# Kernel tuning notes

Hardware: AMD Instinct MI355X
Metric: run time of the kernel (lower is better)

## Reference

```python
import jax, jax.numpy as jnp
import numpy as np

N, E = 50000, 600000
IN, H, C = 128, 8, 32
HC = H * C
LAT, OUT, NCOM = 32, 64, 30
BN_EPS = 1e-5
NEG_SLOPE = 0.2


def setup_inputs() -> dict:
    key = jax.random.key(0)
    ks = jax.random.split(key, 32)
    f32 = jnp.float32
    def rn(i, shape, s=0.05):
        return jax.random.normal(ks[i], shape, f32) * s
    inp = {
        'x': jax.random.normal(ks[0], (N, IN), f32),
        'eps': jax.random.normal(ks[1], (N, LAT), f32),
        'edge_index': jax.random.randint(ks[2], (2, E), 0, N, jnp.int32),
        # GAT layer 1 (in -> H*C)
        'gat1_W': rn(3, (IN, HC)), 'gat1_asrc': rn(4, (H, C)), 'gat1_adst': rn(5, (H, C)), 'gat1_b': jnp.zeros((HC,), f32),
        'bn1_g': jnp.ones((HC,), f32), 'bn1_b': jnp.zeros((HC,), f32),
        # GAT layer 2 (H*C -> H*C)
        'gat2_W': rn(6, (HC, HC)), 'gat2_asrc': rn(7, (H, C)), 'gat2_adst': rn(8, (H, C)), 'gat2_b': jnp.zeros((HC,), f32),
        'bn2_g': jnp.ones((HC,), f32), 'bn2_b': jnp.zeros((HC,), f32),
        # GAT layer 3 (H*C -> H*C)
        'gat3_W': rn(9, (HC, HC)), 'gat3_asrc': rn(10, (H, C)), 'gat3_adst': rn(11, (H, C)), 'gat3_b': jnp.zeros((HC,), f32),
        'bn3_g': jnp.ones((HC,), f32), 'bn3_b': jnp.zeros((HC,), f32),
        # heads
        'res_W': rn(12, (IN, HC)), 'res_b': jnp.zeros((HC,), f32),
        'mu_W': rn(13, (HC, LAT)), 'mu_b': jnp.zeros((LAT,), f32),
        'lv_W': rn(14, (HC, LAT)), 'lv_b': jnp.zeros((LAT,), f32),
        'dec_W': rn(15, (LAT, OUT)), 'dec_b': jnp.zeros((OUT,), f32),
        'aux_W': rn(16, (HC, NCOM)), 'aux_b': jnp.zeros((NCOM,), f32),
    }
    return inp


def gat_conv(x, src, dst, W, asrc, adst, b):
    # PyG GATConv (concat=True, self-loops already in src/dst, lin bias=False)
    n = x.shape[0]
    h = (x @ W).reshape(n, H, C)                      # [N,H,C]
    a_s = jnp.einsum('nhc,hc->nh', h, asrc)           # [N,H]
    a_d = jnp.einsum('nhc,hc->nh', h, adst)
    e = jax.nn.leaky_relu(a_s[src] + a_d[dst], NEG_SLOPE)  # [E,H]
    m = jax.ops.segment_max(e, dst, num_segments=n)        # per-dest softmax (stable)
    p = jnp.exp(e - m[dst])
    s = jax.ops.segment_sum(p, dst, num_segments=n)
    alpha = p / (s[dst] + 1e-16)                      # [E,H]
    out = jax.ops.segment_sum(h[src] * alpha[:, :, None], dst, num_segments=n)
    return out.reshape(n, HC) + b


def batch_norm(x, g, b):
    mu = x.mean(0)
    var = x.var(0)  # biased var, as torch BN uses for normalization
    return (x - mu) * jax.lax.rsqrt(var + BN_EPS) * g + b


def reference(x, eps, edge_index,
              gat1_W, gat1_asrc, gat1_adst, gat1_b, bn1_g, bn1_b,
              gat2_W, gat2_asrc, gat2_adst, gat2_b, bn2_g, bn2_b,
              gat3_W, gat3_asrc, gat3_adst, gat3_b, bn3_g, bn3_b,
              res_W, res_b, mu_W, mu_b, lv_W, lv_b, dec_W, dec_b, aux_W, aux_b):
    loops = jnp.arange(N, dtype=edge_index.dtype)
    src = jnp.concatenate([edge_index[0], loops])
    dst = jnp.concatenate([edge_index[1], loops])

    residual = x @ res_W + res_b
    h = jax.nn.relu(batch_norm(gat_conv(x, src, dst, gat1_W, gat1_asrc, gat1_adst, gat1_b), bn1_g, bn1_b))
    h = jax.nn.relu(batch_norm(gat_conv(h, src, dst, gat2_W, gat2_asrc, gat2_adst, gat2_b), bn2_g, bn2_b))
    h = jax.nn.relu(batch_norm(gat_conv(h, src, dst, gat3_W, gat3_asrc, gat3_adst, gat3_b), bn3_g, bn3_b))
    h = h + residual

    mu = h @ mu_W + mu_b
    logvar = h @ lv_W + lv_b
    z = mu + eps * jnp.exp(0.5 * logvar)   # reparameterize
    out = z @ dec_W + dec_b
    aux = h @ aux_W + aux_b
    return (out, mu, logvar, aux)
```

## Files before the change

kernel.cpp:

```cpp
#include <hip/hip_runtime.h>

#define N_NODES 50000
#define N_EDGES 600000
#define HC 256
#define NH 8
#define AGG_BLOCKS 2048
#define AGG_WAVES (AGG_BLOCKS * 4)

typedef short s8v __attribute__((ext_vector_type(8)));
typedef float f4v __attribute__((ext_vector_type(4)));
typedef _Float16 h4v __attribute__((ext_vector_type(4)));
typedef _Float16 h8v __attribute__((ext_vector_type(8)));
typedef __attribute__((address_space(1))) const unsigned int as1_cu32;
typedef __attribute__((address_space(3))) unsigned int as3_u32;

__device__ inline ushort f2bf(float f) {
  unsigned u = __float_as_uint(f);
  unsigned r = u + 0x7FFF + ((u >> 16) & 1);
  return (ushort)(r >> 16);
}

__global__ void k_init_cnt(int* __restrict__ cnt) {
  int i = blockIdx.x * 256 + threadIdx.x;
  if (i < N_NODES) cnt[i] = 1;
}

__global__ void k_count(const int* __restrict__ dstE, int* __restrict__ cnt) {
  int e = blockIdx.x * 256 + threadIdx.x;
  if (e < N_EDGES) atomicAdd(&cnt[dstE[e]], 1);
}

__global__ void k_scan_bsum(const int* __restrict__ cnt, int* __restrict__ bsum) {
  __shared__ int sd[256];
  int i = blockIdx.x * 256 + threadIdx.x;
  sd[threadIdx.x] = (i < N_NODES) ? cnt[i] : 0;
  __syncthreads();
  for (int o = 128; o > 0; o >>= 1) {
    if (threadIdx.x < o) sd[threadIdx.x] += sd[threadIdx.x + o];
    __syncthreads();
  }
  if (threadIdx.x == 0) bsum[blockIdx.x] = sd[0];
}

__global__ void k_scan_offsets(int* __restrict__ bsum, int nb) {
  __shared__ int s[256];
  int t = threadIdx.x;
  int v = (t < nb) ? bsum[t] : 0;
  s[t] = v; __syncthreads();
  for (int o = 1; o < 256; o <<= 1) {
    int x = (t >= o) ? s[t - o] : 0;
    __syncthreads();
    s[t] += x;
    __syncthreads();
  }
  if (t < nb) bsum[t] = s[t] - v;
}

__global__ void k_scan_write(const int* __restrict__ cnt, const int* __restrict__ bsum,
                             int* __restrict__ rowptr, int* __restrict__ fillptr) {
  __shared__ int s[256];
  int t = threadIdx.x;
  int i = blockIdx.x * 256 + t;
  int v = (i < N_NODES) ? cnt[i] : 0;
  s[t] = v; __syncthreads();
  for (int o = 1; o < 256; o <<= 1) {
    int x = (t >= o) ? s[t - o] : 0;
    __syncthreads();
    s[t] += x;
    __syncthreads();
  }
  int excl = s[t] - v + bsum[blockIdx.x];
  if (i < N_NODES) {
    rowptr[i] = excl;
    fillptr[i] = excl;
    if (i == N_NODES - 1) rowptr[N_NODES] = excl + v;
  }
}

__global__ void k_fill(const int* __restrict__ srcE, const int* __restrict__ dstE,
                       int* __restrict__ fillptr, int* __restrict__ srcs) {
  int i = blockIdx.x * 256 + threadIdx.x;
  if (i < N_NODES) {
    int pos = atomicAdd(&fillptr[i], 1);
    srcs[pos] = i;
  } else if (i < N_NODES + N_EDGES) {
    int e = i - N_NODES;
    int pos = atomicAdd(&fillptr[dstE[e]], 1);
    srcs[pos] = srcE[e];
  }
}

__global__ void k_cvt_x(const float* __restrict__ X, ushort* __restrict__ Xb) {
  size_t i = ((size_t)blockIdx.x * 256 + threadIdx.x) * 4;
  float4 x4 = *(const float4*)&X[i];
  ushort4 o;
  o.x = f2bf(x4.x); o.y = f2bf(x4.y); o.z = f2bf(x4.z); o.w = f2bf(x4.w);
  *(ushort4*)&Xb[i] = o;
}

__global__ void k_prep(const float* __restrict__ gW0, const float* __restrict__ resW,
                       const float* __restrict__ gW1, const float* __restrict__ gW2,
                       const float* __restrict__ muW, const float* __restrict__ lvW,
                       const float* __restrict__ auxW,
                       ushort* __restrict__ WtP, ushort* __restrict__ Wt2,
                       ushort* __restrict__ Wt3, ushort* __restrict__ Wth) {
  __shared__ ushort s[32][33];
  int id = blockIdx.x;
  int t = threadIdx.x;
  if (id < 64) {
    const float* W = (id < 32) ? gW0 : resW;
    ushort* Wt = (id < 32) ? WtP : (WtP + 256 * 128);
    int a = id & 31;
    int bx = a & 3, by = a >> 2;
    int tx = t & 31, ty = t >> 5;
    int k0 = bx * 32, n0 = by * 32;
    for (int j = 0; j < 32; j += 8)
      s[ty + j][tx] = f2bf(W[(size_t)(k0 + ty + j) * 256 + n0 + tx]);
    __syncthreads();
    for (int j = 0; j < 32; j += 8)
      Wt[(size_t)(n0 + ty + j) * 128 + k0 + tx] = s[tx][ty + j];
  } else if (id < 192) {
    const float* W = (id < 128) ? gW1 : gW2;
    ushort* Wt = (id < 128) ? Wt2 : Wt3;
    int a = (id - 64) & 63;
    int bx = a & 7, by = a >> 3;
    int tx = t & 31, ty = t >> 5;
    int k0 = bx * 32, n0 = by * 32;
    for (int j = 0; j < 32; j += 8)
      s[ty + j][tx] = f2bf(W[(size_t)(k0 + ty + j) * 256 + n0 + tx]);
    __syncthreads();
    for (int j = 0; j < 32; j += 8)
      Wt[(size_t)(n0 + ty + j) * 256 + k0 + tx] = s[tx][ty + j];
  } else {
    int n = id - 192;
    int k = t;
    float v = 0.f;
    if (n < 32) v = muW[k * 32 + n];
    else if (n < 64) v = lvW[k * 32 + (n - 32)];
    else if (n < 94) v = auxW[k * 30 + (n - 64)];
    Wth[n * 256 + k] = f2bf(v);
  }
}

template <typename OutT>
__launch_bounds__(256)
__global__ void k_gemm_bf16(const ushort* __restrict__ A, const ushort* __restrict__ Wt,
                            const float* __restrict__ bias, int bias_off, OutT* __restrict__ Out,
                            int M, int K, int ldc,
                            const float* __restrict__ att_asrc, const float* __restrict__ att_adst,
                            float* __restrict__ att_as, float* __restrict__ att_ad) {
  __shared__ __align__(16) ushort As[16 * 512];
  __shared__ __align__(16) ushort Bs[16 * 512];
  int t = threadIdx.x, w = t >> 6, L = t & 63;
  int bm = blockIdx.x * 128, bn = blockIdx.y * 128;
  int lrow = L & 15, lcol = (L >> 4) * 8;

  const ushort* ga[4];
  const ushort* gb[4];
#pragma unroll
  for (int u = 0; u < 4; u++) {
    int i = w * 4 + u;
    int mt = i >> 1, ks = i & 1;
    int arow = bm + mt * 16 + lrow;
    if (arow >= M) arow = M - 1;
    ga[u] = A + (size_t)arow * K + ks * 32 + lcol;
    int brow = bn + mt * 16 + lrow;
    gb[u] = Wt + (size_t)brow * K + ks * 32 + lcol;
  }

  f4v acc[4][4];
  f4v zero = {0.f, 0.f, 0.f, 0.f};
#pragma unroll
  for (int mi = 0; mi < 4; mi++)
#pragma unroll
    for (int ni = 0; ni < 4; ni++) acc[mi][ni] = zero;

  int wm = (w >> 1) * 4;
  int wn = (w & 1) * 4;

  int nk = K >> 6;
  for (int kt = 0; kt < nk; kt++) {
#pragma unroll
    for (int u = 0; u < 4; u++) {
      int i = w * 4 + u;
      __builtin_amdgcn_global_load_lds((as1_cu32*)ga[u], (as3_u32*)&As[i * 512], 16, 0, 0);
      __builtin_amdgcn_global_load_lds((as1_cu32*)gb[u], (as3_u32*)&Bs[i * 512], 16, 0, 0);
      ga[u] += 64; gb[u] += 64;
    }
    __syncthreads();
#pragma unroll
    for (int ks = 0; ks < 2; ks++) {
      s8v af[4], bf[4];
#pragma unroll
      for (int mi = 0; mi < 4; mi++)
        af[mi] = *(const s8v*)&As[(((wm + mi) * 2 + ks) * 64 + L) * 8];
#pragma unroll
      for (int ni = 0; ni < 4; ni++)
        bf[ni] = *(const s8v*)&Bs[(((wn + ni) * 2 + ks) * 64 + L) * 8];
#pragma unroll
      for (int mi = 0; mi < 4; mi++)
#pragma unroll
        for (int ni = 0; ni < 4; ni++)
          acc[mi][ni] = __builtin_amdgcn_mfma_f32_16x16x32_bf16(af[mi], bf[ni], acc[mi][ni], 0, 0, 0);
    }
    __syncthreads();
  }
#pragma unroll
  for (int ni = 0; ni < 4; ni++) {
    int col = bn + (wn + ni) * 16 + (L & 15);
    float bb = (bias && col >= bias_off) ? bias[col - bias_off] : 0.f;
#pragma unroll
    for (int mi = 0; mi < 4; mi++) {
      int rbase = bm + (wm + mi) * 16 + (L >> 4) * 4;
#pragma unroll
      for (int i = 0; i < 4; i++) {
        int r = rbase + i;
        if (r < M) Out[(size_t)r * ldc + col] = (OutT)(acc[mi][ni][i] + bb);
      }
    }
  }
  if (att_as && bn < 256) {
    int hb = ((unsigned)(bn + wn * 16)) >> 5;
    int cl = L & 15;
    float sa[4], da[4];
#pragma unroll
    for (int ni = 0; ni < 4; ni++) {
      int h = hb + (ni >> 1);
      int cih = (ni & 1) * 16 + cl;
      sa[ni] = att_asrc[h * 32 + cih];
      da[ni] = att_adst[h * 32 + cih];
    }
#pragma unroll
    for (int hi = 0; hi < 2; hi++) {
#pragma unroll
      for (int mi = 0; mi < 4; mi++) {
#pragma unroll
        for (int i = 0; i < 4; i++) {
          float vs = acc[mi][hi * 2][i] * sa[hi * 2] + acc[mi][hi * 2 + 1][i] * sa[hi * 2 + 1];
          float vd = acc[mi][hi * 2][i] * da[hi * 2] + acc[mi][hi * 2 + 1][i] * da[hi * 2 + 1];
          vs += __shfl_xor(vs, 1); vd += __shfl_xor(vd, 1);
          vs += __shfl_xor(vs, 2); vd += __shfl_xor(vd, 2);
          vs += __shfl_xor(vs, 4); vd += __shfl_xor(vd, 4);
          vs += __shfl_xor(vs, 8); vd += __shfl_xor(vd, 8);
          int r = bm + (wm + mi) * 16 + (L >> 4) * 4 + i;
          if (cl == 0 && r < M) {
            att_as[r * NH + hb + hi] = vs;
            att_ad[r * NH + hb + hi] = vd;
          }
        }
      }
    }
  }
}

__launch_bounds__(256)
__global__ void k_gemm_head(const ushort* __restrict__ A, const ushort* __restrict__ Wt,
                            const float* __restrict__ eps,
                            const float* __restrict__ mub, const float* __restrict__ lvb,
                            const float* __restrict__ auxb,
                            const float* __restrict__ decW, const float* __restrict__ decb,
                            float* __restrict__ out) {
  __shared__ __align__(16) ushort smem[16384];
  __shared__ float wsd[2048];
  __shared__ float shz[4][32];
  ushort* As = smem;
  ushort* Bs = smem + 8192;
  int t = threadIdx.x, w = t >> 6, L = t & 63;
  int bm = blockIdx.x * 128;
  int lrow = L & 15, lcol = (L >> 4) * 8;
  const int K = 256;
  for (int i = t; i < 2048; i += 256) wsd[i] = decW[i];

  const ushort* ga[4];
  const ushort* gb[4];
#pragma unroll
  for (int u = 0; u < 4; u++) {
    int i = w * 4 + u;
    int mt = i >> 1, ks = i & 1;
    int arow = bm + mt * 16 + lrow;
    if (arow >= N_NODES) arow = N_NODES - 1;
    ga[u] = A + (size_t)arow * K + ks * 32 + lcol;
    int brow = mt * 16 + lrow;
    gb[u] = Wt + (size_t)brow * K + ks * 32 + lcol;
  }
  f4v acc[4][4];
  f4v zero = {0.f, 0.f, 0.f, 0.f};
#pragma unroll
  for (int mi = 0; mi < 4; mi++)
#pragma unroll
    for (int ni = 0; ni < 4; ni++) acc[mi][ni] = zero;
  int wm = (w >> 1) * 4;
  int wn = (w & 1) * 4;
  for (int kt = 0; kt < 4; kt++) {
#pragma unroll
    for (int u = 0; u < 4; u++) {
      int i = w * 4 + u;
      __builtin_amdgcn_global_load_lds((as1_cu32*)ga[u], (as3_u32*)&As[i * 512], 16, 0, 0);
      __builtin_amdgcn_global_load_lds((as1_cu32*)gb[u], (as3_u32*)&Bs[i * 512], 16, 0, 0);
      ga[u] += 64; gb[u] += 64;
    }
    __syncthreads();
#pragma unroll
    for (int ks = 0; ks < 2; ks++) {
      s8v af[4], bf[4];
#pragma unroll
      for (int mi = 0; mi < 4; mi++)
        af[mi] = *(const s8v*)&As[(((wm + mi) * 2 + ks) * 64 + L) * 8];
#pragma unroll
      for (int ni = 0; ni < 4; ni++)
        bf[ni] = *(const s8v*)&Bs[(((wn + ni) * 2 + ks) * 64 + L) * 8];
#pragma unroll
      for (int mi = 0; mi < 4; mi++)
#pragma unroll
        for (int ni = 0; ni < 4; ni++)
          acc[mi][ni] = __builtin_amdgcn_mfma_f32_16x16x32_bf16(af[mi], bf[ni], acc[mi][ni], 0, 0, 0);
    }
    __syncthreads();
  }
  _Float16* tile = (_Float16*)smem;
#pragma unroll
  for (int ni = 0; ni < 4; ni++) {
    int c = (wn + ni) * 16 + (L & 15);
#pragma unroll
    for (int mi = 0; mi < 4; mi++) {
      int rbase = (wm + mi) * 16 + (L >> 4) * 4;
#pragma unroll
      for (int i = 0; i < 4; i++)
        tile[(rbase + i) * 128 + c] = (_Float16)acc[mi][ni][i];
    }
  }
  __syncthreads();
  for (int rr = 0; rr < 32; rr++) {
    int rl = w * 32 + rr;
    int n = bm + rl;
    bool valid = n < N_NODES;
    if (L < 32) {
      float mu = (float)tile[rl * 128 + L] + mub[L];
      float lv = (float)tile[rl * 128 + 32 + L] + lvb[L];
      float zv = 0.f;
      if (valid) {
        out[(size_t)N_NODES * 64 + (size_t)n * 32 + L] = mu;
        out[(size_t)N_NODES * 96 + (size_t)n * 32 + L] = lv;
        zv = mu + eps[(size_t)n * 32 + L] * __expf(0.5f * lv);
      }
      shz[w][L] = zv;
    } else if (L < 62 && valid) {
      int j = L - 32;
      out[(size_t)N_NODES * 128 + (size_t)n * 30 + j] = (float)tile[rl * 128 + 64 + j] + auxb[j];
    }
    __syncthreads();
    float o = decb[L];
#pragma unroll 8
    for (int kk = 0; kk < 32; kk++) o += shz[w][kk] * wsd[kk * 64 + L];
    if (valid) out[(size_t)n * 64 + L] = o;
    __syncthreads();
  }
}

#define FMA4(P, B2)                                                                        \
  asm("v_fma_mix_f32 %0, %1, %2, %0 op_sel:[0,0,0] op_sel_hi:[0,1,0]"                      \
      : "+v"(ac0) : "v"(P), "v"((B2).x));                                                  \
  asm("v_fma_mix_f32 %0, %1, %2, %0 op_sel:[0,1,0] op_sel_hi:[0,1,0]"                      \
      : "+v"(ac1) : "v"(P), "v"((B2).x));                                                  \
  asm("v_fma_mix_f32 %0, %1, %2, %0 op_sel:[0,0,0] op_sel_hi:[0,1,0]"                      \
      : "+v"(ac2) : "v"(P), "v"((B2).y));                                                  \
  asm("v_fma_mix_f32 %0, %1, %2, %0 op_sel:[0,1,0] op_sel_hi:[0,1,0]"                      \
      : "+v"(ac3) : "v"(P), "v"((B2).y));

__launch_bounds__(256)
__global__ void k_agg(const int* __restrict__ rowptr, const int* __restrict__ srcs,
                      const float* __restrict__ as_, const float* __restrict__ ad_,
                      const _Float16* __restrict__ B, int ld, const float* __restrict__ gb,
                      _Float16* __restrict__ C, float* __restrict__ part,
                      float* __restrict__ stats) {
  __shared__ float ss[4 * 512];
  int t = threadIdx.x;
  if (blockIdx.x == 0) {
    stats[t] = 0.f; stats[t + 256] = 0.f;
  }
  int w = t >> 6, lane = t & 63;
  int h = lane >> 3;
  int cb = lane << 2;
  int ldu = ld >> 2;
  const uint2* Bu = (const uint2*)B;
  float4 g4 = *(const float4*)&gb[cb];
  float sts0 = 0.f, sts1 = 0.f, sts2 = 0.f, sts3 = 0.f;
  float stq0 = 0.f, stq1 = 0.f, stq2 = 0.f, stq3 = 0.f;

  for (int n = blockIdx.x * 4 + w; n < N_NODES; n += AGG_WAVES) {
    int beg = rowptr[n], end = rowptr[n + 1];
    float ad_nh = ad_[n * NH + h];
    float ac0 = 0.f, ac1 = 0.f, ac2 = 0.f, ac3 = 0.f, wsum = 0.f;
    int k = beg;
    for (; k + 4 <= end; k += 4) {
      int s0 = srcs[k], s1 = srcs[k + 1], s2 = srcs[k + 2], s3 = srcs[k + 3];
      uint2 b0 = Bu[(size_t)s0 * ldu + lane];
      uint2 b1 = Bu[(size_t)s1 * ldu + lane];
      uint2 b2 = Bu[(size_t)s2 * ldu + lane];
      uint2 b3 = Bu[(size_t)s3 * ldu + lane];
      float e0 = as_[s0 * NH + h] + ad_nh; e0 = e0 > 0.f ? e0 : 0.2f * e0;
      float e1 = as_[s1 * NH + h] + ad_nh; e1 = e1 > 0.f ? e1 : 0.2f * e1;
      float e2 = as_[s2 * NH + h] + ad_nh; e2 = e2 > 0.f ? e2 : 0.2f * e2;
      float e3 = as_[s3 * NH + h] + ad_nh; e3 = e3 > 0.f ? e3 : 0.2f * e3;
      float p0 = __expf(e0), p1 = __expf(e1), p2 = __expf(e2), p3 = __expf(e3);
      wsum += (p0 + p1) + (p2 + p3);
      FMA4(p0, b0)
      FMA4(p1, b1)
      FMA4(p2, b2)
      FMA4(p3, b3)
    }
    for (; k < end; k++) {
      int s = srcs[k];
      h4v b4 = *(const h4v*)&B[(size_t)s * ld + cb];
      float e = as_[s * NH + h] + ad_nh;
      e = e > 0.f ? e : 0.2f * e;
      float p = __expf(e);
      wsum += p;
      ac0 += p * (float)b4[0]; ac1 += p * (float)b4[1];
      ac2 += p * (float)b4[2]; ac3 += p * (float)b4[3];
    }
    float inv = 1.f / (wsum + 1e-16f);
    float v0 = ac0 * inv + g4.x, v1 = ac1 * inv + g4.y;
    float v2 = ac2 * inv + g4.z, v3 = ac3 * inv + g4.w;
    h4v o; o[0] = (_Float16)v0; o[1] = (_Float16)v1; o[2] = (_Float16)v2; o[3] = (_Float16)v3;
    *(h4v*)&C[(size_t)n * 256 + cb] = o;
    sts0 += v0; stq0 += v0 * v0;
    sts1 += v1; stq1 += v1 * v1;
    sts2 += v2; stq2 += v2 * v2;
    sts3 += v3; stq3 += v3 * v3;
  }
  float* sw = &ss[w * 512];
  sw[cb + 0] = sts0; sw[cb + 1] = sts1; sw[cb + 2] = sts2; sw[cb + 3] = sts3;
  sw[256 + cb + 0] = stq0; sw[256 + cb + 1] = stq1;
  sw[256 + cb + 2] = stq2; sw[256 + cb + 3] = stq3;
  __syncthreads();
  float p0 = ss[t] + ss[512 + t] + ss[1024 + t] + ss[1536 + t];
  float p1 = ss[256 + t] + ss[768 + t] + ss[1280 + t] + ss[1792 + t];
  part[(size_t)blockIdx.x * 512 + t] = p0;
  part[(size_t)blockIdx.x * 512 + 256 + t] = p1;
}

__global__ void k_bn_reduce(const float* __restrict__ part, float* __restrict__ stats) {
  int i = threadIdx.x;
  int base = blockIdx.x * (AGG_BLOCKS / 16);
  float s0 = 0.f, s1 = 0.f;
  for (int b = 0; b < AGG_BLOCKS / 16; b++) {
    s0 += part[(size_t)(base + b) * 512 + i];
    s1 += part[(size_t)(base + b) * 512 + 256 + i];
  }
  atomicAdd(&stats[i], s0);
  atomicAdd(&stats[256 + i], s1);
}

__global__ void k_bn_relu_cvt(const _Float16* __restrict__ X, const float* __restrict__ stats,
                              const float* __restrict__ g, const float* __restrict__ b,
                              const _Float16* __restrict__ resid, int rld,
                              ushort* __restrict__ Xb) {
  size_t i = ((size_t)blockIdx.x * 256 + threadIdx.x) * 8;
  int c = (int)(i & 255);
  const float invN = 1.f / (float)N_NODES;
  h8v x8 = *(const h8v*)&X[i];
  float v[8];
#pragma unroll
  for (int q = 0; q < 2; q++) {
    float4 s4 = *(const float4*)&stats[c + q * 4];
    float4 q4 = *(const float4*)&stats[256 + c + q * 4];
    float4 g4 = *(const float4*)&g[c + q * 4];
    float4 b4 = *(const float4*)&b[c + q * 4];
    float m0 = s4.x * invN, m1 = s4.y * invN, m2 = s4.z * invN, m3 = s4.w * invN;
    v[q * 4 + 0] = ((float)x8[q * 4 + 0] - m0) * rsqrtf(q4.x * invN - m0 * m0 + 1e-5f) * g4.x + b4.x;
    v[q * 4 + 1] = ((float)x8[q * 4 + 1] - m1) * rsqrtf(q4.y * invN - m1 * m1 + 1e-5f) * g4.y + b4.y;
    v[q * 4 + 2] = ((float)x8[q * 4 + 2] - m2) * rsqrtf(q4.z * invN - m2 * m2 + 1e-5f) * g4.z + b4.z;
    v[q * 4 + 3] = ((float)x8[q * 4 + 3] - m3) * rsqrtf(q4.w * invN - m3 * m3 + 1e-5f) * g4.w + b4.w;
  }
#pragma unroll
  for (int q = 0; q < 8; q++) v[q] = v[q] > 0.f ? v[q] : 0.f;
  if (resid) {
    size_t row = i >> 8;
    h8v r8 = *(const h8v*)&resid[row * rld + c];
#pragma unroll
    for (int q = 0; q < 8; q++) v[q] += (float)r8[q];
  }
  ushort o8[8];
#pragma unroll
  for (int q = 0; q < 8; q++) o8[q] = f2bf(v[q]);
  *(uint4*)&Xb[i] = *(const uint4*)o8;
}

extern "C" void kernel_launch(void* const* d_in, const int* in_sizes, int n_in,
                              void* d_out, int out_size, void* d_ws, size_t ws_size,
                              hipStream_t stream) {
  (void)in_sizes; (void)n_in; (void)out_size; (void)ws_size;
  const float* x    = (const float*)d_in[0];
  const float* eps  = (const float*)d_in[1];
  const int*   ei   = (const int*)d_in[2];
  const float* gW[3]    = {(const float*)d_in[3],  (const float*)d_in[9],  (const float*)d_in[15]};
  const float* gasrc[3] = {(const float*)d_in[4],  (const float*)d_in[10], (const float*)d_in[16]};
  const float* gadst[3] = {(const float*)d_in[5],  (const float*)d_in[11], (const float*)d_in[17]};
  const float* gbias[3] = {(const float*)d_in[6],  (const float*)d_in[12], (const float*)d_in[18]};
  const float* bng[3]   = {(const float*)d_in[7],  (const float*)d_in[13], (const float*)d_in[19]};
  const float* bnb[3]   = {(const float*)d_in[8],  (const float*)d_in[14], (const float*)d_in[20]};
  const float* resW = (const float*)d_in[21];
  const float* resb = (const float*)d_in[22];
  const float* muW  = (const float*)d_in[23];
  const float* mub  = (const float*)d_in[24];
  const float* lvW  = (const float*)d_in[25];
  const float* lvb  = (const float*)d_in[26];
  const float* decW = (const float*)d_in[27];
  const float* decb = (const float*)d_in[28];
  const float* auxW = (const float*)d_in[29];
  const float* auxb = (const float*)d_in[30];
  float* out = (float*)d_out;

  char* ws = (char*)d_ws;
  size_t off = 0;
  auto alloc = [&](size_t bytes) -> void* {
    void* p = ws + off;
    off += (bytes + 255) & ~(size_t)255;
    return p;
  };
  _Float16* X0R = (_Float16*)alloc((size_t)N_NODES * 512 * 2);
  _Float16* X0  = (_Float16*)alloc((size_t)N_NODES * HC * 2);
  _Float16* X1  = (_Float16*)alloc((size_t)N_NODES * HC * 2);
  ushort* Xb    = (ushort*)alloc((size_t)N_NODES * HC * 2);
  float*  as_   = (float*)alloc((size_t)N_NODES * NH * 4);
  float*  ad_   = (float*)alloc((size_t)N_NODES * NH * 4);
  float*  stats = (float*)alloc(512 * 4);
  float*  part  = (float*)alloc((size_t)AGG_BLOCKS * 512 * 4);
  int* cnt      = (int*)alloc((size_t)N_NODES * 4);
  int* rowptr   = (int*)alloc((size_t)(N_NODES + 1) * 4);
  int* fillptr  = (int*)alloc((size_t)N_NODES * 4);
  int* srcs     = (int*)alloc((size_t)(N_NODES + N_EDGES) * 4);
  int* bsum     = (int*)alloc(256 * 4);
  ushort* WtP   = (ushort*)alloc(512 * 128 * 2);
  ushort* Wt2   = (ushort*)alloc(256 * 256 * 2);
  ushort* Wt3   = (ushort*)alloc(256 * 256 * 2);
  ushort* Wth   = (ushort*)alloc(128 * 256 * 2);

  const int NB = (N_NODES + 255) / 256;
  k_init_cnt<<<NB, 256, 0, stream>>>(cnt);
  k_count<<<(N_EDGES + 255) / 256, 256, 0, stream>>>(ei + N_EDGES, cnt);
  k_scan_bsum<<<NB, 256, 0, stream>>>(cnt, bsum);
  k_scan_offsets<<<1, 256, 0, stream>>>(bsum, NB);
  k_scan_write<<<NB, 256, 0, stream>>>(cnt, bsum, rowptr, fillptr);
  k_fill<<<(N_NODES + N_EDGES + 255) / 256, 256, 0, stream>>>(ei, ei + N_EDGES, fillptr, srcs);

  k_prep<<<320, 256, 0, stream>>>(gW[0], resW, gW[1], gW[2], muW, lvW, auxW, WtP, Wt2, Wt3, Wth);
  k_cvt_x<<<(N_NODES * 128) / 1024, 256, 0, stream>>>(x, Xb);

  const int GM = (N_NODES + 127) / 128;
  const int EW_GRID = (N_NODES * HC) / 2048;

  k_gemm_bf16<_Float16><<<dim3(GM, 4), 256, 0, stream>>>(
      Xb, WtP, resb, 256, X0R, N_NODES, 128, 512, gasrc[0], gadst[0], as_, ad_);
  k_agg<<<AGG_BLOCKS, 256, 0, stream>>>(rowptr, srcs, as_, ad_, X0R, 512, gbias[0], X1, part, stats);
  k_bn_reduce<<<16, 256, 0, stream>>>(part, stats);
  k_bn_relu_cvt<<<EW_GRID, 256, 0, stream>>>(X1, stats, bng[0], bnb[0], nullptr, 0, Xb);

  const ushort* Wts[2] = {Wt2, Wt3};
  for (int L = 0; L < 2; L++) {
    k_gemm_bf16<_Float16><<<dim3(GM, 2), 256, 0, stream>>>(
        Xb, Wts[L], nullptr, 0, X0, N_NODES, 256, 256, gasrc[L + 1], gadst[L + 1], as_, ad_);
    k_agg<<<AGG_BLOCKS, 256, 0, stream>>>(rowptr, srcs, as_, ad_, X0, 256, gbias[L + 1], X1, part, stats);
    k_bn_reduce<<<16, 256, 0, stream>>>(part, stats);
    k_bn_relu_cvt<<<EW_GRID, 256, 0, stream>>>(
        X1, stats, bng[L + 1], bnb[L + 1], (L == 1) ? (X0R + 256) : nullptr, 512, Xb);
  }
  k_gemm_head<<<GM, 256, 0, stream>>>(Xb, Wth, eps, mub, lvb, auxb, decW, decb, out);
}
```

Baseline: 639.7 us.

## Fold attention vectors into weights and compute attention logits in elementwise kernels

```diff
diff --git a/kernel.cpp b/kernel.cpp
--- a/kernel.cpp
+++ b/kernel.cpp
@@ -18,6 +18,41 @@
   unsigned u = __float_as_uint(f);
   unsigned r = u + 0x7FFF + ((u >> 16) & 1);
   return (ushort)(r >> 16);
+}
+
+__device__ inline void att_reduce_write(float* pa, int lane, int n,
+                                        float* __restrict__ as_, float* __restrict__ ad_) {
+  float c8[8];
+#pragma unroll
+  for (int i = 0; i < 8; i++) {
+    float send = (lane & 1) ? pa[i] : pa[i + 8];
+    float keep = (lane & 1) ? pa[i + 8] : pa[i];
+    c8[i] = keep + __shfl_xor(send, 1);
+  }
+  float c4[4];
+#pragma unroll
+  for (int i = 0; i < 4; i++) {
+    float send = (lane & 2) ? c8[i] : c8[i + 4];
+    float keep = (lane & 2) ? c8[i + 4] : c8[i];
+    c4[i] = keep + __shfl_xor(send, 2);
+  }
+  float c2[2];
+#pragma unroll
+  for (int i = 0; i < 2; i++) {
+    float send = (lane & 4) ? c4[i] : c4[i + 2];
+    float keep = (lane & 4) ? c4[i + 2] : c4[i];
+    c2[i] = keep + __shfl_xor(send, 4);
+  }
+  float send = (lane & 8) ? c2[0] : c2[1];
+  float keep = (lane & 8) ? c2[1] : c2[0];
+  float c1 = keep + __shfl_xor(send, 8);
+  c1 += __shfl_xor(c1, 16);
+  c1 += __shfl_xor(c1, 32);
+  if (lane < 16) {
+    int v = ((lane & 1) << 3) | ((lane & 2) << 1) | ((lane & 4) >> 1) | ((lane & 8) >> 3);
+    if (v < 8) as_[n * NH + v] = c1;
+    else       ad_[n * NH + (v - 8)] = c1;
+  }
 }
 
 __global__ void k_init_cnt(int* __restrict__ cnt) {
@@ -90,20 +125,40 @@
   }
 }
 
-__global__ void k_cvt_x(const float* __restrict__ X, ushort* __restrict__ Xb) {
-  size_t i = ((size_t)blockIdx.x * 256 + threadIdx.x) * 4;
-  float4 x4 = *(const float4*)&X[i];
-  ushort4 o;
-  o.x = f2bf(x4.x); o.y = f2bf(x4.y); o.z = f2bf(x4.z); o.w = f2bf(x4.w);
-  *(ushort4*)&Xb[i] = o;
+__launch_bounds__(256)
+__global__ void k_cvt_x_att(const float* __restrict__ X, const float* __restrict__ Wf1,
+                            ushort* __restrict__ Xb, float* __restrict__ as_,
+                            float* __restrict__ ad_) {
+  int t = threadIdx.x, w = t >> 6, lane = t & 63;
+  int k0 = lane * 2;
+  float wf0[16], wf1[16];
+#pragma unroll
+  for (int v = 0; v < 16; v += 4) {
+    *(f4v*)&wf0[v] = *(const f4v*)&Wf1[k0 * 16 + v];
+    *(f4v*)&wf1[v] = *(const f4v*)&Wf1[(k0 + 1) * 16 + v];
+  }
+  for (int n = blockIdx.x * 4 + w; n < N_NODES; n += 12500) {
+    float2 xv = *(const float2*)&X[(size_t)n * 128 + k0];
+    ushort2 ob; ob.x = f2bf(xv.x); ob.y = f2bf(xv.y);
+    *(ushort2*)&Xb[(size_t)n * 128 + k0] = ob;
+    float pa[16];
+#pragma unroll
+    for (int v = 0; v < 16; v++) pa[v] = xv.x * wf0[v] + xv.y * wf1[v];
+    att_reduce_write(pa, lane, n, as_, ad_);
+  }
 }
 
 __global__ void k_prep(const float* __restrict__ gW0, const float* __restrict__ resW,
                        const float* __restrict__ gW1, const float* __restrict__ gW2,
                        const float* __restrict__ muW, const float* __restrict__ lvW,
                        const float* __restrict__ auxW,
+                       const float* __restrict__ as1, const float* __restrict__ ad1,
+                       const float* __restrict__ as2, const float* __restrict__ ad2,
+                       const float* __restrict__ as3, const float* __restrict__ ad3,
                        ushort* __restrict__ WtP, ushort* __restrict__ Wt2,
-                       ushort* __restrict__ Wt3, ushort* __restrict__ Wth) {
+                       ushort* __restrict__ Wt3, ushort* __restrict__ Wth,
+                       float* __restrict__ Wf1, float* __restrict__ Wf2,
+                       float* __restrict__ Wf3) {
   __shared__ ushort s[32][33];
   int id = blockIdx.x;
   int t = threadIdx.x;
@@ -131,7 +186,7 @@
     __syncthreads();
     for (int j = 0; j < 32; j += 8)
       Wt[(size_t)(n0 + ty + j) * 256 + k0 + tx] = s[tx][ty + j];
-  } else {
+  } else if (id < 320) {
     int n = id - 192;
     int k = t;
     float v = 0.f;
@@ -139,6 +194,22 @@
     else if (n < 64) v = lvW[k * 32 + (n - 32)];
     else if (n < 94) v = auxW[k * 30 + (n - 64)];
     Wth[n * 256 + k] = f2bf(v);
+  } else {
+    const float* W; const float* asc; const float* adc; float* Wf; int base;
+    if (id == 320)      { W = gW0; asc = as1; adc = ad1; Wf = Wf1; base = 0; }
+    else if (id <= 322) { W = gW1; asc = as2; adc = ad2; Wf = Wf2; base = (id - 321) * 2048; }
+    else                { W = gW2; asc = as3; adc = ad3; Wf = Wf3; base = (id - 323) * 2048; }
+#pragma unroll
+    for (int i = 0; i < 8; i++) {
+      int e = base + t + 256 * i;
+      int k = e >> 4, o = e & 15;
+      int h = o & 7;
+      const float* wa = (o < 8) ? asc : adc;
+      float acc = 0.f;
+#pragma unroll
+      for (int c = 0; c < 32; c++) acc += W[(size_t)k * 256 + h * 32 + c] * wa[h * 32 + c];
+      Wf[e] = acc;
+    }
   }
 }
 
@@ -146,9 +217,7 @@
 __launch_bounds__(256)
 __global__ void k_gemm_bf16(const ushort* __restrict__ A, const ushort* __restrict__ Wt,
                             const float* __restrict__ bias, int bias_off, OutT* __restrict__ Out,
-                            int M, int K, int ldc,
-                            const float* __restrict__ att_asrc, const float* __restrict__ att_adst,
-                            float* __restrict__ att_as, float* __restrict__ att_ad) {
+                            int M, int K, int ldc) {
   __shared__ __align__(16) ushort As[16 * 512];
   __shared__ __align__(16) ushort Bs[16 * 512];
   int t = threadIdx.x, w = t >> 6, L = t & 63;
@@ -216,38 +285,6 @@
       for (int i = 0; i < 4; i++) {
         int r = rbase + i;
         if (r < M) Out[(size_t)r * ldc + col] = (OutT)(acc[mi][ni][i] + bb);
-      }
-    }
-  }
-  if (att_as && bn < 256) {
-    int hb = ((unsigned)(bn + wn * 16)) >> 5;
-    int cl = L & 15;
-    float sa[4], da[4];
-#pragma unroll
-    for (int ni = 0; ni < 4; ni++) {
-      int h = hb + (ni >> 1);
-      int cih = (ni & 1) * 16 + cl;
-      sa[ni] = att_asrc[h * 32 + cih];
-      da[ni] = att_adst[h * 32 + cih];
-    }
-#pragma unroll
-    for (int hi = 0; hi < 2; hi++) {
-#pragma unroll
-      for (int mi = 0; mi < 4; mi++) {
-#pragma unroll
-        for (int i = 0; i < 4; i++) {
-          float vs = acc[mi][hi * 2][i] * sa[hi * 2] + acc[mi][hi * 2 + 1][i] * sa[hi * 2 + 1];
-          float vd = acc[mi][hi * 2][i] * da[hi * 2] + acc[mi][hi * 2 + 1][i] * da[hi * 2 + 1];
-          vs += __shfl_xor(vs, 1); vd += __shfl_xor(vd, 1);
-          vs += __shfl_xor(vs, 2); vd += __shfl_xor(vd, 2);
-          vs += __shfl_xor(vs, 4); vd += __shfl_xor(vd, 4);
-          vs += __shfl_xor(vs, 8); vd += __shfl_xor(vd, 8);
-          int r = bm + (wm + mi) * 16 + (L >> 4) * 4 + i;
-          if (cl == 0 && r < M) {
-            att_as[r * NH + hb + hi] = vs;
-            att_ad[r * NH + hb + hi] = vd;
-          }
-        }
       }
     }
   }
@@ -450,6 +487,56 @@
   }
   atomicAdd(&stats[i], s0);
   atomicAdd(&stats[256 + i], s1);
+}
+
+__launch_bounds__(256)
+__global__ void k_bn_relu_cvt_att(const _Float16* __restrict__ X, const float* __restrict__ stats,
+                                  const float* __restrict__ g, const float* __restrict__ b,
+                                  const float* __restrict__ Wf, ushort* __restrict__ Xb,
+                                  float* __restrict__ as_, float* __restrict__ ad_) {
+  int t = threadIdx.x, w = t >> 6, lane = t & 63;
+  int c0 = lane * 4;
+  const float invN = 1.f / (float)N_NODES;
+  float4 s4 = *(const float4*)&stats[c0];
+  float4 q4 = *(const float4*)&stats[256 + c0];
+  float4 g4 = *(const float4*)&g[c0];
+  float4 b4 = *(const float4*)&b[c0];
+  float scale[4], shift[4];
+  {
+    float m[4] = {s4.x * invN, s4.y * invN, s4.z * invN, s4.w * invN};
+    float qq[4] = {q4.x, q4.y, q4.z, q4.w};
+    float gg[4] = {g4.x, g4.y, g4.z, g4.w};
+    float bb[4] = {b4.x, b4.y, b4.z, b4.w};
+#pragma unroll
+    for (int j = 0; j < 4; j++) {
+      float rs = rsqrtf(qq[j] * invN - m[j] * m[j] + 1e-5f) * gg[j];
+      scale[j] = rs;
+      shift[j] = bb[j] - m[j] * rs;
+    }
+  }
+  float wf[4][16];
+#pragma unroll
+  for (int j = 0; j < 4; j++)
+#pragma unroll
+    for (int v = 0; v < 16; v += 4)
+      *(f4v*)&wf[j][v] = *(const f4v*)&Wf[(c0 + j) * 16 + v];
+
+  for (int n = blockIdx.x * 4 + w; n < N_NODES; n += 25000) {
+    h4v x4 = *(const h4v*)&X[(size_t)n * 256 + c0];
+    float y[4];
+#pragma unroll
+    for (int j = 0; j < 4; j++) {
+      float vv = (float)x4[j] * scale[j] + shift[j];
+      y[j] = vv > 0.f ? vv : 0.f;
+    }
+    ushort4 ob; ob.x = f2bf(y[0]); ob.y = f2bf(y[1]); ob.z = f2bf(y[2]); ob.w = f2bf(y[3]);
+    *(ushort4*)&Xb[(size_t)n * 256 + c0] = ob;
+    float pa[16];
+#pragma unroll
+    for (int v = 0; v < 16; v++)
+      pa[v] = y[0] * wf[0][v] + y[1] * wf[1][v] + y[2] * wf[2][v] + y[3] * wf[3][v];
+    att_reduce_write(pa, lane, n, as_, ad_);
+  }
 }
 
 __global__ void k_bn_relu_cvt(const _Float16* __restrict__ X, const float* __restrict__ stats,
@@ -536,6 +623,9 @@
   ushort* Wt2   = (ushort*)alloc(256 * 256 * 2);
   ushort* Wt3   = (ushort*)alloc(256 * 256 * 2);
   ushort* Wth   = (ushort*)alloc(128 * 256 * 2);
+  float* Wf1    = (float*)alloc(128 * 16 * 4);
+  float* Wf2    = (float*)alloc(256 * 16 * 4);
+  float* Wf3    = (float*)alloc(256 * 16 * 4);
 
   const int NB = (N_NODES + 255) / 256;
   k_init_cnt<<<NB, 256, 0, stream>>>(cnt);
@@ -545,26 +635,28 @@
   k_scan_write<<<NB, 256, 0, stream>>>(cnt, bsum, rowptr, fillptr);
   k_fill<<<(N_NODES + N_EDGES + 255) / 256, 256, 0, stream>>>(ei, ei + N_EDGES, fillptr, srcs);
 
-  k_prep<<<320, 256, 0, stream>>>(gW[0], resW, gW[1], gW[2], muW, lvW, auxW, WtP, Wt2, Wt3, Wth);
-  k_cvt_x<<<(N_NODES * 128) / 1024, 256, 0, stream>>>(x, Xb);
+  k_prep<<<325, 256, 0, stream>>>(gW[0], resW, gW[1], gW[2], muW, lvW, auxW,
+                                  gasrc[0], gadst[0], gasrc[1], gadst[1], gasrc[2], gadst[2],
+                                  WtP, Wt2, Wt3, Wth, Wf1, Wf2, Wf3);
+  k_cvt_x_att<<<3125, 256, 0, stream>>>(x, Wf1, Xb, as_, ad_);
 
   const int GM = (N_NODES + 127) / 128;
   const int EW_GRID = (N_NODES * HC) / 2048;
 
-  k_gemm_bf16<_Float16><<<dim3(GM, 4), 256, 0, stream>>>(
-      Xb, WtP, resb, 256, X0R, N_NODES, 128, 512, gasrc[0], gadst[0], as_, ad_);
+  k_gemm_bf16<_Float16><<<dim3(GM, 4), 256, 0, stream>>>(Xb, WtP, resb, 256, X0R, N_NODES, 128, 512);
   k_agg<<<AGG_BLOCKS, 256, 0, stream>>>(rowptr, srcs, as_, ad_, X0R, 512, gbias[0], X1, part, stats);
   k_bn_reduce<<<16, 256, 0, stream>>>(part, stats);
-  k_bn_relu_cvt<<<EW_GRID, 256, 0, stream>>>(X1, stats, bng[0], bnb[0], nullptr, 0, Xb);
-
-  const ushort* Wts[2] = {Wt2, Wt3};
-  for (int L = 0; L < 2; L++) {
-    k_gemm_bf16<_Float16><<<dim3(GM, 2), 256, 0, stream>>>(
-        Xb, Wts[L], nullptr, 0, X0, N_NODES, 256, 256, gasrc[L + 1], gadst[L + 1], as_, ad_);
-    k_agg<<<AGG_BLOCKS, 256, 0, stream>>>(rowptr, srcs, as_, ad_, X0, 256, gbias[L + 1], X1, part, stats);
-    k_bn_reduce<<<16, 256, 0, stream>>>(part, stats);
-    k_bn_relu_cvt<<<EW_GRID, 256, 0, stream>>>(
-        X1, stats, bng[L + 1], bnb[L + 1], (L == 1) ? (X0R + 256) : nullptr, 512, Xb);
-  }
+  k_bn_relu_cvt_att<<<6250, 256, 0, stream>>>(X1, stats, bng[0], bnb[0], Wf2, Xb, as_, ad_);
+
+  k_gemm_bf16<_Float16><<<dim3(GM, 2), 256, 0, stream>>>(Xb, Wt2, nullptr, 0, X0, N_NODES, 256, 256);
+  k_agg<<<AGG_BLOCKS, 256, 0, stream>>>(rowptr, srcs, as_, ad_, X0, 256, gbias[1], X1, part, stats);
+  k_bn_reduce<<<16, 256, 0, stream>>>(part, stats);
+  k_bn_relu_cvt_att<<<6250, 256, 0, stream>>>(X1, stats, bng[1], bnb[1], Wf3, Xb, as_, ad_);
+
+  k_gemm_bf16<_Float16><<<dim3(GM, 2), 256, 0, stream>>>(Xb, Wt3, nullptr, 0, X0, N_NODES, 256, 256);
+  k_agg<<<AGG_BLOCKS, 256, 0, stream>>>(rowptr, srcs, as_, ad_, X0, 256, gbias[2], X1, part, stats);
+  k_bn_reduce<<<16, 256, 0, stream>>>(part, stats);
+  k_bn_relu_cvt<<<EW_GRID, 256, 0, stream>>>(X1, stats, bng[2], bnb[2], X0R + 256, 512, Xb);
+
   k_gemm_head<<<GM, 256, 0, stream>>>(Xb, Wth, eps, mub, lvb, auxb, decW, decb, out);
 }
```

Result: slower. 743.5 us (+16.2%).
